# Kernel tuning notes

Measured on AMD Instinct MI355X. Metric: run time of the kernel, lower is better.

Reference implementation:

```python
import jax, jax.numpy as jnp
import numpy as np
from jax import lax

B, TX, TY = 32, 512, 1024
D, H, FN, KS, L = 256, 2, 1024, 9, 4
WORD_NUM = 256
NEG = -1e9


def sinusoid_table(seq_len, d):
    pos = np.arange(seq_len)[:, None].astype(np.float64)
    i = np.arange(d)[None, :]
    angle = pos / np.power(10000.0, 2 * (i // 2) / d)
    table = np.zeros((seq_len, d))
    table[:, 0::2] = np.sin(angle[:, 0::2])
    table[:, 1::2] = np.cos(angle[:, 1::2])
    return jnp.asarray(table, dtype=jnp.float32)


def setup_inputs():
    key = jax.random.key(0)
    ks = jax.random.split(key, 16)
    s = 0.02
    w = lambda k, shape: jax.random.normal(k, shape, jnp.float32) * s
    embed = w(ks[4], (WORD_NUM, D)).at[0].set(0.0)  # padding_idx=0
    return dict(
        tokens=jax.random.randint(ks[0], (B, TX), 1, WORD_NUM),
        src_lengths=jax.random.randint(ks[1], (B,), TX // 2, TX + 1),
        mel_lengths=jax.random.randint(ks[2], (B,), TY // 2, TY + 1),
        value=jax.random.normal(ks[3], (B, TX, TY), jnp.float32),
        embed=embed,
        pos_enc=sinusoid_table(TX, D),
        wq=w(ks[5], (L, D, D)), bq=jnp.zeros((L, D), jnp.float32),
        wk=w(ks[6], (L, D, D)), bk=jnp.zeros((L, D), jnp.float32),
        wv=w(ks[7], (L, D, D)), bv=jnp.zeros((L, D), jnp.float32),
        wo=w(ks[8], (L, D, D)), bo=jnp.zeros((L, D), jnp.float32),
        ln1_g=jnp.ones((L, D), jnp.float32), ln1_b=jnp.zeros((L, D), jnp.float32),
        c1_w=w(ks[9], (L, FN, D, KS)), c1_b=jnp.zeros((L, FN), jnp.float32),
        c2_w=w(ks[10], (L, D, FN, KS)), c2_b=jnp.zeros((L, D), jnp.float32),
        ln2_g=jnp.ones((L, D), jnp.float32), ln2_b=jnp.zeros((L, D), jnp.float32),
    )


def layer_norm(x, g, b, eps=1e-5):
    m = jnp.mean(x, axis=-1, keepdims=True)
    v = jnp.mean(jnp.square(x - m), axis=-1, keepdims=True)
    return (x - m) * lax.rsqrt(v + eps) * g + b


def conv1d(x, w, b):
    # x: [B, C_in, T], w: [C_out, C_in, K]
    p = (w.shape[-1] - 1) // 2
    y = lax.conv_general_dilated(x, w, (1,), [(p, p)],
                                 dimension_numbers=('NCH', 'OIH', 'NCH'))
    return y + b[None, :, None]


def maximum_path(value, mask):
    # Monotonic alignment search DP. value, mask: [B, Tx, Ty]
    b, tx, ty = value.shape
    value = value * mask
    x_range = jnp.arange(tx)[None, :]

    def fwd_step(v, inp):
        j, val_j = inp
        v0 = jnp.concatenate([jnp.full((b, 1), NEG, value.dtype), v[:, :-1]], axis=1)
        max_mask = v >= v0
        v_max = jnp.where(max_mask, v, v0)
        v_new = jnp.where(x_range <= j, v_max + val_j, NEG)
        return v_new, max_mask

    _, directions = lax.scan(fwd_step, jnp.zeros((b, tx), value.dtype),
                             (jnp.arange(ty), jnp.moveaxis(value, 2, 0)))
    directions = jnp.where(jnp.moveaxis(mask, 2, 0).astype(bool), directions, True)

    idx0 = mask[:, :, 0].sum(1).astype(jnp.int32) - 1  # last valid x index per batch
    brange = jnp.arange(b)

    def bwd_step(idx, dir_j):
        col = jax.nn.one_hot(idx, tx, dtype=value.dtype)
        idx_new = idx + dir_j[brange, idx].astype(jnp.int32) - 1
        return idx_new, col

    _, cols = lax.scan(bwd_step, idx0, directions, reverse=True)
    path = jnp.moveaxis(cols, 0, 2) * mask  # [B, Tx, Ty]
    return path


def reference(tokens, src_lengths, mel_lengths, value, embed, pos_enc,
              wq, bq, wk, bk, wv, bv, wo, bo, ln1_g, ln1_b,
              c1_w, c1_b, c2_w, c2_b, ln2_g, ln2_b):
    bsz, tx = tokens.shape
    pad = jnp.arange(tx)[None, :] >= src_lengths[:, None]      # [B,Tx] True=pad
    mel_pad = jnp.arange(TY)[None, :] >= mel_lengths[:, None]  # [B,Ty]
    dk = D // H
    scale = 1.0 / np.sqrt(dk).astype(np.float32)

    x = embed[tokens] + pos_enc[None, :tx, :]
    for l in range(L):
        # --- multi-head self-attention ---
        res = x
        q = (x @ wq[l] + bq[l]).reshape(bsz, tx, H, dk)
        k = (x @ wk[l] + bk[l]).reshape(bsz, tx, H, dk)
        v = (x @ wv[l] + bv[l]).reshape(bsz, tx, H, dk)
        attn = jnp.einsum('bqhd,bkhd->bhqk', q, k) * scale
        attn = jnp.where(pad[:, None, None, :], NEG, attn)
        attn = jax.nn.softmax(attn, axis=-1)
        out = jnp.einsum('bhqk,bkhd->bqhd', attn, v).reshape(bsz, tx, D)
        x = layer_norm(out @ wo[l] + bo[l] + res, ln1_g[l], ln1_b[l])
        x = jnp.where(pad[:, :, None], 0.0, x)
        # --- conv1d FFN ---
        res = x
        h = x.transpose(0, 2, 1)
        h = jax.nn.relu(conv1d(h, c1_w[l], c1_b[l]))
        h = conv1d(h, c2_w[l], c2_b[l]).transpose(0, 2, 1)
        x = layer_norm(h + res, ln2_g[l], ln2_b[l])
        x = jnp.where(pad[:, :, None], 0.0, x)

    mas_mask = ((~pad)[:, :, None] & (~mel_pad)[:, None, :]).astype(jnp.float32)
    path = maximum_path(value, mas_mask)                 # [B,Tx,Ty]
    expanded = jnp.einsum('bxy,bxd->byd', path, x)       # [B,Ty,D]
    return expanded
```

## Files before the change

kernel.cpp:

```cpp
#include <hip/hip_runtime.h>

#define B_  32
#define TX  512
#define TY  1024
#define D_  256
#define H_  2
#define DK  128
#define FN  1024
#define NL  4
#define TXP 520
#define NEGF (-1e9f)

typedef __attribute__((ext_vector_type(4))) float f32x4;
typedef __attribute__((ext_vector_type(8))) short short8;
typedef __attribute__((ext_vector_type(4))) unsigned short ushort4v;

typedef __attribute__((address_space(3))) unsigned int lds_u32;
typedef __attribute__((address_space(1))) const unsigned int glb_u32;

__device__ __forceinline__ unsigned short f2bf(float x) {
  unsigned int u = __builtin_bit_cast(unsigned int, x);
  u += 0x7fffu + ((u >> 16) & 1u);
  return (unsigned short)(u >> 16);
}
__device__ __forceinline__ float bf2f(unsigned short x) {
  unsigned int u = ((unsigned int)x) << 16;
  return __builtin_bit_cast(float, u);
}
__device__ __forceinline__ void store_bf16x4(unsigned short* p, f32x4 v) {
  ushort4v o; o[0]=f2bf(v[0]); o[1]=f2bf(v[1]); o[2]=f2bf(v[2]); o[3]=f2bf(v[3]);
  *(ushort4v*)p = o;
}
__device__ __forceinline__ float wsum(float v) {
#pragma unroll
  for (int i = 1; i < 64; i <<= 1) v += __shfl_xor(v, i, 64);
  return v;
}
__device__ __forceinline__ float wmax(float v) {
#pragma unroll
  for (int i = 1; i < 64; i <<= 1) v = fmaxf(v, __shfl_xor(v, i, 64));
  return v;
}
__device__ __forceinline__ void gl_lds16(const unsigned short* g, unsigned short* l) {
  __builtin_amdgcn_global_load_lds((glb_u32*)g, (lds_u32*)l, 16, 0, 0);
}
__device__ __forceinline__ void gl_lds16f(const float* g, float* l) {
  __builtin_amdgcn_global_load_lds((glb_u32*)g, (lds_u32*)l, 16, 0, 0);
}
__device__ __forceinline__ float lane_shr1(float x) {
  int r = __builtin_amdgcn_update_dpp(0, __builtin_bit_cast(int, x), 0x138, 0xF, 0xF, false);
  return __builtin_bit_cast(float, r);
}

static const size_t OFF_XB   = 0;
static const size_t SZ_XB    = (size_t)B_*TXP*D_*2;
static const size_t OFF_HB   = OFF_XB + SZ_XB;
static const size_t SZ_HB    = (size_t)B_*TXP*FN*2;
static const size_t OFF_QKV  = OFF_HB + SZ_HB;
static const size_t SZ_QKV   = (size_t)B_*TX*768*2;
static const size_t OFF_S    = OFF_QKV + SZ_QKV;
static const size_t SZ_S     = (size_t)B_*H_*TX*TX*2;
static const size_t OFF_AO   = OFF_S + SZ_S;
static const size_t SZ_AO    = (size_t)B_*TX*D_*2;
static const size_t OFF_T1   = OFF_AO + SZ_AO;
static const size_t SZ_T1    = (size_t)B_*TX*D_*4;
static const size_t OFF_WQKV = OFF_T1 + SZ_T1;
static const size_t SZ_WQKV  = (size_t)NL*768*256*2;
static const size_t OFF_BQKV = OFF_WQKV + SZ_WQKV;
static const size_t SZ_BQKV  = (size_t)NL*768*4;
static const size_t OFF_WO   = OFF_BQKV + SZ_BQKV;
static const size_t SZ_WO    = (size_t)NL*256*256*2;
static const size_t OFF_WT1  = OFF_WO + SZ_WO;
static const size_t SZ_WT1   = (size_t)NL*9*1024*256*2;
static const size_t OFF_WT2  = OFF_WT1 + SZ_WT1;
static const size_t SZ_WT2   = SZ_WT1;
static const size_t OFF_DIRS = OFF_WT2 + SZ_WT2;
static const size_t SZ_DIRS  = (size_t)B_*TY*64;
static const size_t OFF_IDX  = OFF_DIRS + SZ_DIRS;

__global__ void repack_qkvw(const float* __restrict__ wq, const float* __restrict__ wk,
                            const float* __restrict__ wv, unsigned short* __restrict__ out) {
  int i = blockIdx.x*256 + threadIdx.x;
  if (i >= NL*768*256) return;
  int c = i & 255, j = (i >> 8) % 768, l = i / (768*256);
  const float* src = (j < 256) ? wq : (j < 512) ? wk : wv;
  out[i] = f2bf(src[((size_t)l*256 + c)*256 + (j & 255)]);
}
__global__ void repack_bias(const float* __restrict__ bq, const float* __restrict__ bk,
                            const float* __restrict__ bv, float* __restrict__ out) {
  int i = blockIdx.x*256 + threadIdx.x;
  if (i >= NL*768) return;
  int j = i % 768, l = i / 768;
  const float* src = (j < 256) ? bq : (j < 512) ? bk : bv;
  out[i] = src[l*256 + (j & 255)];
}
__global__ void repack_wo(const float* __restrict__ wo, unsigned short* __restrict__ out) {
  int i = blockIdx.x*256 + threadIdx.x;
  if (i >= NL*256*256) return;
  int c = i & 255, j = (i >> 8) & 255, l = i >> 16;
  out[i] = f2bf(wo[((size_t)l*256 + c)*256 + j]);
}
__global__ void repack_c1(const float* __restrict__ w, unsigned short* __restrict__ out) {
  int i = blockIdx.x*256 + threadIdx.x;
  if (i >= NL*9*1024*256) return;
  int c = i & 255; int rest = i >> 8;
  int f = rest & 1023; int rest2 = rest >> 10;
  int k = rest2 % 9, l = rest2 / 9;
  out[i] = f2bf(w[(((size_t)l*1024 + f)*256 + c)*9 + k]);
}
__global__ void repack_c2(const float* __restrict__ w, unsigned short* __restrict__ out) {
  int i = blockIdx.x*256 + threadIdx.x;
  if (i >= NL*9*256*1024) return;
  int f = i & 1023; int rest = i >> 10;
  int d = rest & 255; int rest2 = rest >> 8;
  int k = rest2 % 9, l = rest2 / 9;
  out[i] = f2bf(w[(((size_t)l*256 + d)*1024 + f)*9 + k]);
}
__global__ void zero_halo(unsigned short* __restrict__ xb, unsigned short* __restrict__ hb) {
  int i = blockIdx.x*256 + threadIdx.x;
  if (i < 65536) {
    int b = i >> 11, r = (i >> 8) & 7, c = i & 255;
    int row = (r < 4) ? r : (512 + r);
    xb[((size_t)b*TXP + row)*256 + c] = 0;
  } else {
    int j = i - 65536;
    if (j < 262144) {
      int b = j >> 13, r = (j >> 10) & 7, c = j & 1023;
      int row = (r < 4) ? r : (512 + r);
      hb[((size_t)b*TXP + row)*1024 + c] = 0;
    }
  }
}

__global__ __launch_bounds__(256) void embed_kernel(const int* __restrict__ tok,
    const float* __restrict__ emb, const float* __restrict__ pos,
    unsigned short* __restrict__ xbo ) {
  int row = blockIdx.x*4 + (threadIdx.x >> 6);
  int t = row & 511, b = row >> 9;
  int lane = threadIdx.x & 63;
  int tk = tok[row];
  f32x4 e = *(const f32x4*)(emb + (size_t)tk*256 + lane*4);
  f32x4 p = *(const f32x4*)(pos + (size_t)t*256 + lane*4);
  f32x4 v;
#pragma unroll
  for (int i = 0; i < 4; i++) v[i] = e[i] + p[i];
  store_bf16x4(xbo + ((size_t)b*TXP + t)*256 + lane*4, v);
}

__global__ __launch_bounds__(256) void gemm_mfma(
    const unsigned short* __restrict__ A, long long AbO, long long AhO, int Astr,
    const unsigned short* __restrict__ W, long long WbO, long long WhO, int Wstr,
    const float* __restrict__ bias,
    float* __restrict__ O32, long long O32bO, int O32str,
    unsigned short* __restrict__ O16, long long O16bO, long long O16hO, int O16str,
    int Cin, int Cout, int ks, int relu, int H,
    const int* __restrict__ sl, float scale, int maskmode) {
  __shared__ unsigned short As[136*32];
  __shared__ unsigned short Ws[2*128*32];
  const int tid = threadIdx.x;
  int b, h;
  if (H == 2) { b = blockIdx.z >> 1; h = blockIdx.z & 1; }
  else        { b = blockIdx.z;      h = 0; }
  const int t0 = blockIdx.x * 128;
  const int f0 = blockIdx.y * 128;
  const unsigned short* Ab = A + (size_t)b * AbO + (size_t)h * AhO;
  const unsigned short* Wb = W + (size_t)b * WbO + (size_t)h * WhO;
  const int lane = tid & 63, w = tid >> 6;
  const int wt = (w & 1) << 6, wf = (w >> 1) << 6;
  const int lr = lane & 15, lh = lane >> 4;
  const int r0 = tid >> 2, cg = (tid & 3) << 3;
  f32x4 zed = {0.f, 0.f, 0.f, 0.f};
  f32x4 acc[4][4];
#pragma unroll
  for (int i = 0; i < 4; i++)
#pragma unroll
    for (int j = 0; j < 4; j++) acc[i][j] = zed;

  for (int c0 = 0; c0 < Cin; c0 += 32) {
    __syncthreads();
    gl_lds16(Ab + (size_t)(t0 + r0) * Astr + (c0 + cg),         As + (size_t)tid * 8);
    gl_lds16(Ab + (size_t)(t0 + r0 + 64) * Astr + (c0 + cg),    As + (size_t)(tid + 256) * 8);
    if (ks > 1 && tid < 32)
      gl_lds16(Ab + (size_t)(t0 + r0 + 128) * Astr + (c0 + cg), As + (size_t)(tid + 512) * 8);
    {
      const unsigned short* W0 = Wb + (size_t)f0 * Wstr;
      gl_lds16(W0 + (size_t)r0 * Wstr + (c0 + cg),        Ws + (size_t)tid * 8);
      gl_lds16(W0 + (size_t)(r0 + 64) * Wstr + (c0 + cg), Ws + (size_t)(tid + 256) * 8);
    }
    for (int k = 0; k < ks; ++k) {
      __syncthreads();
      if (k + 1 < ks) {
        const unsigned short* Wn = Wb + ((size_t)(k + 1) * Cout + f0) * Wstr;
        unsigned short* Wd = Ws + (size_t)((k + 1) & 1) * 4096;
        gl_lds16(Wn + (size_t)r0 * Wstr + (c0 + cg),        Wd + (size_t)tid * 8);
        gl_lds16(Wn + (size_t)(r0 + 64) * Wstr + (c0 + cg), Wd + (size_t)(tid + 256) * 8);
      }
      const unsigned short* Wsk = Ws + (size_t)(k & 1) * 4096;
      short8 af[4], bfv[4];
#pragma unroll
      for (int mt = 0; mt < 4; mt++) af[mt]  = *(const short8*)&As[(k + wt + mt*16 + lr)*32 + lh*8];
#pragma unroll
      for (int nt = 0; nt < 4; nt++) bfv[nt] = *(const short8*)&Wsk[(wf + nt*16 + lr)*32 + lh*8];
#pragma unroll
      for (int mt = 0; mt < 4; mt++)
#pragma unroll
        for (int nt = 0; nt < 4; nt++)
          acc[mt][nt] = __builtin_amdgcn_mfma_f32_16x16x32_bf16(af[mt], bfv[nt], acc[mt][nt], 0, 0, 0);
    }
  }
  const int slb = maskmode ? sl[b] : 0;
#pragma unroll
  for (int mt = 0; mt < 4; mt++) {
    int trow = t0 + wt + mt*16 + lh*4;
#pragma unroll
    for (int nt = 0; nt < 4; nt++) {
      int f = f0 + wf + nt*16 + lr;
      float bb = (!maskmode && bias) ? bias[f] : 0.f;
#pragma unroll
      for (int r = 0; r < 4; r++) {
        float v;
        if (maskmode) {
          v = acc[mt][nt][r] * scale;
          if (f >= slb) v = NEGF;
        } else {
          v = acc[mt][nt][r] + bb;
          if (relu) v = fmaxf(v, 0.f);
        }
        if (O32) O32[(size_t)b*O32bO + (size_t)(trow + r)*O32str + f] = v;
        if (O16) O16[(size_t)b*O16bO + (size_t)h*O16hO + (size_t)(trow + r)*O16str + f] = f2bf(v);
      }
    }
  }
}

__global__ __launch_bounds__(256) void vtrans_kernel(const unsigned short* __restrict__ qkv,
    unsigned short* __restrict__ VT) {
  const int z = blockIdx.z, b = z >> 1, h = z & 1;
  const int t0 = blockIdx.x << 5, d0 = blockIdx.y << 5;
  __shared__ unsigned short tile[32][33];
  const int tx = threadIdx.x, ty = threadIdx.y;
  const unsigned short* src = qkv + (size_t)b*TX*768 + 512 + h*DK;
#pragma unroll
  for (int i = 0; i < 4; i++)
    tile[ty + i*8][tx] = src[(size_t)(t0 + ty + i*8)*768 + d0 + tx];
  __syncthreads();
#pragma unroll
  for (int i = 0; i < 4; i++)
    VT[((size_t)z*DK + d0 + ty + i*8)*512 + t0 + tx] = tile[tx][ty + i*8];
}

__global__ __launch_bounds__(256) void softmax_kernel(unsigned short* __restrict__ S) {
  const int row = blockIdx.x*4 + (threadIdx.x >> 6);
  const int lane = threadIdx.x & 63;
  unsigned short* p = S + (size_t)row*512 + lane*8;
  short8 raw = *(const short8*)p;
  float a[8];
#pragma unroll
  for (int i = 0; i < 8; i++) a[i] = bf2f((unsigned short)raw[i]);
  float m = a[0];
#pragma unroll
  for (int i = 1; i < 8; i++) m = fmaxf(m, a[i]);
  m = wmax(m);
  float s = 0.f;
#pragma unroll
  for (int i = 0; i < 8; i++) { a[i] = __expf(a[i]-m); s += a[i]; }
  s = wsum(s);
  float inv = 1.f / s;
  short8 o;
#pragma unroll
  for (int i = 0; i < 8; i++) o[i] = (short)f2bf(a[i] * inv);
  *(short8*)p = o;
}

__global__ __launch_bounds__(256) void ln_kernel(const float* __restrict__ tin,
    const float* __restrict__ g, const float* __restrict__ bt, const int* __restrict__ sl,
    unsigned short* __restrict__ xbo ) {
  const int row = blockIdx.x*4 + (threadIdx.x >> 6);
  const int b = row >> 9, t = row & 511;
  const int lane = threadIdx.x & 63;
  unsigned short* xp = xbo + ((size_t)b*TXP + t)*256 + lane*4;
  f32x4 tv = *(const f32x4*)(tin + (size_t)row*256 + lane*4);
  ushort4v rv4 = *(const ushort4v*)xp;
  f32x4 s; float su = 0.f, sq = 0.f;
#pragma unroll
  for (int i = 0; i < 4; i++) {
    s[i] = tv[i] + bf2f(rv4[i]);
    su += s[i]; sq += s[i]*s[i];
  }
  su = wsum(su); sq = wsum(sq);
  float mean = su * (1.f/256.f);
  float var = fmaxf(sq * (1.f/256.f) - mean*mean, 0.f);
  float rs = rsqrtf(var + 1e-5f);
  f32x4 gg = *(const f32x4*)(g + lane*4);
  f32x4 bb = *(const f32x4*)(bt + lane*4);
  bool padr = (t >= sl[b]);
  f32x4 y;
#pragma unroll
  for (int i = 0; i < 4; i++) {
    float yy = (s[i]-mean)*rs*gg[i] + bb[i];
    y[i] = padr ? 0.f : yy;
  }
  store_bf16x4(xp, y);
}

__global__ __launch_bounds__(256) void transpose_mask(const float* __restrict__ value,
    const int* __restrict__ sl, const int* __restrict__ ml, float* __restrict__ vT) {
  const int b = blockIdx.z;
  const int x0 = blockIdx.y << 5, y0 = blockIdx.x << 5;
  __shared__ float tile[32][33];
  const int tx = threadIdx.x, ty = threadIdx.y;
  const int slb = sl[b], mlb = ml[b];
#pragma unroll
  for (int i = 0; i < 4; i++) {
    int x = x0 + ty + i*8, y = y0 + tx;
    float v = value[((size_t)b*TX + x)*TY + y];
    tile[ty + i*8][tx] = (x < slb && y < mlb) ? v : 0.f;
  }
  __syncthreads();
#pragma unroll
  for (int i = 0; i < 4; i++) {
    int y = y0 + ty + i*8, x = x0 + tx;
    vT[((size_t)b*TY + y)*TX + x] = tile[tx][ty + i*8];
  }
}

template<bool RAMP>
__device__ __forceinline__ void dp_comp8(
    int jb, const float* valbuf, unsigned long long* dll,
    float v[8], int lane, int xbase, unsigned int vmask, unsigned int fmask,
    bool lane0) {
  unsigned int w0 = 0, w1 = 0;
#pragma unroll
  for (int u = 0; u < 8; ++u) {
    const int j = jb*8 + u;
    f32x4 a0 = *(const f32x4*)(valbuf + u*512 + lane*8);
    f32x4 a1 = *(const f32x4*)(valbuf + u*512 + lane*8 + 4);
    float vp = lane_shr1(v[7]);
    if (lane0) vp = NEGF;
    unsigned int ge = 0;
#pragma unroll
    for (int i = 7; i >= 1; --i) {
      unsigned int g = (v[i] >= v[i-1]) ? 1u : 0u;
      ge = (ge << 1) | g;
      float nv = fmaxf(v[i], v[i-1]) + ((i < 4) ? a0[i] : a1[i-4]);
      if (RAMP) v[i] = (xbase + i <= j) ? nv : NEGF;
      else      v[i] = nv;
    }
    {
      unsigned int g = (v[0] >= vp) ? 1u : 0u;
      ge = (ge << 1) | g;
      float nv = fmaxf(v[0], vp) + a0[0];
      if (RAMP) v[0] = (xbase <= j) ? nv : NEGF;
      else      v[0] = nv;
    }
    unsigned int byt = (ge & vmask) | fmask;
    if (u < 4) w0 |= byt << (8*u); else w1 |= byt << (8*(u-4));
  }
  dll[jb*64 + lane] = ((unsigned long long)w1 << 32) | w0;
}

__global__ __launch_bounds__(64, 1) void dp_fused(const float* __restrict__ vT,
    const int* __restrict__ sl, const int* __restrict__ ml,
    int* __restrict__ idxout) {
  __shared__ float sval[3*4096];
  __shared__ unsigned long long dll[TY*8];
  unsigned char* dld = (unsigned char*)dll;
  const int b = blockIdx.x, lane = threadIdx.x;
  const int slb = sl[b], mlb = ml[b];
  const float* vb = vT + (size_t)b*TY*TX;
  const int xbase = lane*8;
  const bool lane0 = (lane == 0);
  unsigned int vmaskv = 0;
#pragma unroll
  for (int i = 0; i < 8; ++i) if (xbase + i < slb) vmaskv |= (1u << i);
  const unsigned int fmaskv = (~vmaskv) & 0xffu;
  float v[8];
#pragma unroll
  for (int i = 0; i < 8; ++i) v[i] = 0.f;
  const int jbEnd = (mlb + 7) >> 3;

  auto stage = [&](int jb, float* buf) {
    const float* src = vb + (size_t)jb*8*TX;
#pragma unroll
    for (int u = 0; u < 8; ++u) {
      gl_lds16f(src + u*TX + lane*4,       buf + u*512);
      gl_lds16f(src + u*TX + 256 + lane*4, buf + u*512 + 256);
    }
  };
  stage(0, sval);
  stage(1, sval + 4096);
  stage(2, sval + 8192);
  int buf = 0;
  int jb = 0;
  for (; jb < 64; ++jb) {
    if (jb + 2 < jbEnd)      asm volatile("s_waitcnt vmcnt(32)" ::: "memory");
    else if (jb + 1 < jbEnd) asm volatile("s_waitcnt vmcnt(16)" ::: "memory");
    else                     asm volatile("s_waitcnt vmcnt(0)"  ::: "memory");
    float* vbuf = sval + buf*4096;
    dp_comp8<true>(jb, vbuf, dll, v, lane, xbase, vmaskv, fmaskv, lane0);
    __builtin_amdgcn_sched_barrier(0);
    if (jb + 3 < jbEnd) stage(jb + 3, vbuf);
    buf = (buf == 2) ? 0 : buf + 1;
  }
  for (; jb < jbEnd; ++jb) {
    if (jb + 2 < jbEnd)      asm volatile("s_waitcnt vmcnt(32)" ::: "memory");
    else if (jb + 1 < jbEnd) asm volatile("s_waitcnt vmcnt(16)" ::: "memory");
    else                     asm volatile("s_waitcnt vmcnt(0)"  ::: "memory");
    float* vbuf = sval + buf*4096;
    dp_comp8<false>(jb, vbuf, dll, v, lane, xbase, vmaskv, fmaskv, lane0);
    __builtin_amdgcn_sched_barrier(0);
    if (jb + 3 < jbEnd) stage(jb + 3, vbuf);
    buf = (buf == 2) ? 0 : buf + 1;
  }
  for (int jj = mlb + lane; jj < TY; jj += 64) idxout[b*TY + jj] = -1;
  if (lane0) {
    int* ob = idxout + b*TY;
    int idx = slb - 1;
    int j = mlb - 1;
    while (j >= 6) {
      int o0 = idx >> 3;
      int o1 = (o0 > 0) ? (o0 - 1) : 0;
      unsigned int bc[7], ba[7];
#pragma unroll
      for (int s = 0; s < 7; ++s) {
        int r = j - s;
        int rbase = ((r >> 3) << 9) + (r & 7);
        bc[s] = dld[rbase + o0*8];
        ba[s] = dld[rbase + o1*8];
      }
#pragma unroll
      for (int s = 0; s < 7; ++s) {
        ob[j - s] = idx;
        unsigned int byt = ((idx >> 3) == o0) ? bc[s] : ba[s];
        idx += (int)((byt >> (idx & 7)) & 1u) - 1;
      }
      j -= 7;
    }
    while (j >= 0) {
      ob[j] = idx;
      unsigned int byt = dld[((j >> 3) << 9) + (j & 7) + (idx >> 3)*8];
      idx += (int)((byt >> (idx & 7)) & 1u) - 1;
      --j;
    }
  }
}

__global__ __launch_bounds__(256) void gather_kernel(const unsigned short* __restrict__ xbo,
    const int* __restrict__ idxout, float* __restrict__ out) {
  const int row = blockIdx.x*4 + (threadIdx.x >> 6);
  const int lane = threadIdx.x & 63;
  const int b = row >> 10;
  const int idx = idxout[row];
  f32x4 v;
  if (idx >= 0) {
    ushort4v r = *(const ushort4v*)(xbo + ((size_t)b*TXP + idx)*256 + lane*4);
#pragma unroll
    for (int i = 0; i < 4; i++) v[i] = bf2f(r[i]);
  } else { v[0]=0.f; v[1]=0.f; v[2]=0.f; v[3]=0.f; }
  *(f32x4*)(out + (size_t)row*256 + lane*4) = v;
}

extern "C" void kernel_launch(void* const* d_in, const int* in_sizes, int n_in,
                              void* d_out, int out_size, void* d_ws, size_t ws_size,
                              hipStream_t stream) {
  const int*   tokens = (const int*)d_in[0];
  const int*   sl     = (const int*)d_in[1];
  const int*   ml     = (const int*)d_in[2];
  const float* value  = (const float*)d_in[3];
  const float* emb    = (const float*)d_in[4];
  const float* pos    = (const float*)d_in[5];
  const float* wq     = (const float*)d_in[6];
  const float* bq     = (const float*)d_in[7];
  const float* wk     = (const float*)d_in[8];
  const float* bk     = (const float*)d_in[9];
  const float* wv     = (const float*)d_in[10];
  const float* bv     = (const float*)d_in[11];
  const float* wo     = (const float*)d_in[12];
  const float* bo     = (const float*)d_in[13];
  const float* ln1g   = (const float*)d_in[14];
  const float* ln1bb  = (const float*)d_in[15];
  const float* c1w    = (const float*)d_in[16];
  const float* c1b    = (const float*)d_in[17];
  const float* c2w    = (const float*)d_in[18];
  const float* c2b    = (const float*)d_in[19];
  const float* ln2g   = (const float*)d_in[20];
  const float* ln2bb  = (const float*)d_in[21];

  char* w8 = (char*)d_ws;
  unsigned short* xb     = (unsigned short*)(w8 + OFF_XB);
  unsigned short* hb     = (unsigned short*)(w8 + OFF_HB);
  unsigned short* qkvb   = (unsigned short*)(w8 + OFF_QKV);
  unsigned short* S      = (unsigned short*)(w8 + OFF_S);
  float*          vT     = (float*)(w8 + OFF_HB);
  unsigned short* VT     = (unsigned short*)(w8 + OFF_T1);
  unsigned short* ao     = (unsigned short*)(w8 + OFF_AO);
  float*          T1     = (float*)(w8 + OFF_T1);
  unsigned short* wqkv_r = (unsigned short*)(w8 + OFF_WQKV);
  float*          bqkv   = (float*)(w8 + OFF_BQKV);
  unsigned short* wo_r   = (unsigned short*)(w8 + OFF_WO);
  unsigned short* wt1r   = (unsigned short*)(w8 + OFF_WT1);
  unsigned short* wt2r   = (unsigned short*)(w8 + OFF_WT2);
  int*            idxout = (int*)(w8 + OFF_IDX);
  float*          out    = (float*)d_out;

  const float scale = 0.08838834764831843f;

  repack_qkvw<<<(NL*768*256 + 255)/256, 256, 0, stream>>>(wq, wk, wv, wqkv_r);
  repack_bias<<<(NL*768 + 255)/256, 256, 0, stream>>>(bq, bk, bv, bqkv);
  repack_wo<<<(NL*256*256 + 255)/256, 256, 0, stream>>>(wo, wo_r);
  repack_c1<<<(NL*9*1024*256 + 255)/256, 256, 0, stream>>>(c1w, wt1r);
  repack_c2<<<(NL*9*256*1024 + 255)/256, 256, 0, stream>>>(c2w, wt2r);

  transpose_mask<<<dim3(32, 16, 32), dim3(32, 8), 0, stream>>>(value, sl, ml, vT);
  dp_fused<<<32, 64, 0, stream>>>(vT, sl, ml, idxout);

  zero_halo<<<(327680 + 255)/256, 256, 0, stream>>>(xb, hb);
  embed_kernel<<<4096, 256, 0, stream>>>(tokens, emb, pos, xb + 4*256);

  for (int l = 0; l < NL; l++) {
    gemm_mfma<<<dim3(4, 6, 32), 256, 0, stream>>>(
        xb + 4*256, (long long)TXP*256, 0, 256,
        wqkv_r + (size_t)l*768*256, 0, 0, 256,
        bqkv + l*768,
        nullptr, 0, 0,
        qkvb, (long long)TX*768, 0, 768,
        256, 768, 1, 0, 1, nullptr, 0.f, 0);
    gemm_mfma<<<dim3(4, 4, 64), 256, 0, stream>>>(
        qkvb, (long long)TX*768, 128, 768,
        qkvb + 256, (long long)TX*768, 128, 768,
        nullptr,
        nullptr, 0, 0,
        S, (long long)2*512*512, (long long)512*512, 512,
        128, 512, 1, 0, 2, sl, scale, 1);
    softmax_kernel<<<8192, 256, 0, stream>>>(S);
    vtrans_kernel<<<dim3(16, 4, 64), dim3(32, 8), 0, stream>>>(qkvb, VT);
    gemm_mfma<<<dim3(4, 1, 64), 256, 0, stream>>>(
        S, (long long)2*512*512, (long long)512*512, 512,
        VT, (long long)2*DK*512, (long long)DK*512, 512,
        nullptr,
        nullptr, 0, 0,
        ao, (long long)TX*256, 128, 256,
        512, 128, 1, 0, 2, nullptr, 0.f, 0);
    gemm_mfma<<<dim3(4, 2, 32), 256, 0, stream>>>(
        ao, (long long)TX*256, 0, 256,
        wo_r + (size_t)l*256*256, 0, 0, 256,
        bo + l*256,
        T1, (long long)TX*256, 256,
        nullptr, 0, 0, 0,
        256, 256, 1, 0, 1, nullptr, 0.f, 0);
    ln_kernel<<<4096, 256, 0, stream>>>(T1, ln1g + l*256, ln1bb + l*256, sl, xb + 4*256);
    gemm_mfma<<<dim3(4, 8, 32), 256, 0, stream>>>(
        xb, (long long)TXP*256, 0, 256,
        wt1r + (size_t)l*9*1024*256, 0, 0, 256,
        c1b + l*1024,
        nullptr, 0, 0,
        hb + 4*1024, (long long)TXP*1024, 0, 1024,
        256, 1024, 9, 1, 1, nullptr, 0.f, 0);
    gemm_mfma<<<dim3(4, 2, 32), 256, 0, stream>>>(
        hb, (long long)TXP*1024, 0, 1024,
        wt2r + (size_t)l*9*256*1024, 0, 0, 1024,
        c2b + l*256,
        T1, (long long)TX*256, 256,
        nullptr, 0, 0, 0,
        1024, 256, 9, 0, 1, nullptr, 0.f, 0);
    ln_kernel<<<4096, 256, 0, stream>>>(T1, ln2g + l*256, ln2bb + l*256, sl, xb + 4*256);
  }

  gather_kernel<<<8192, 256, 0, stream>>>(xb + 4*256, idxout, out);
  (void)in_sizes; (void)n_in; (void)out_size; (void)ws_size;
}
```

Measured before the change: 2.050 ms.

## Skip padded row tiles and masked key tiles in MFMA GEMMs

Adds a per-batch skip in the GEMM kernel so 128-row tiles past the source length (plus a conv halo margin) exit early. In mask mode, key tiles entirely beyond the length skip the K loop and write NEG directly. The conv loop order is changed to iterate taps outermost and reload the shifted A tile per tap instead of reusing an extended tile, which drops W double-buffering and raises global/LDS traffic for the conv GEMMs. Padded V columns are zeroed and qkvb is memset once so skipped rows hold defined values, at the risk of stale data in other skipped outputs (T1, hb rows) that later kernels might read.

```diff
diff --git a/kernel.cpp b/kernel.cpp
--- a/kernel.cpp
+++ b/kernel.cpp
@@ -154,15 +154,18 @@
     float* __restrict__ O32, long long O32bO, int O32str,
     unsigned short* __restrict__ O16, long long O16bO, long long O16hO, int O16str,
     int Cin, int Cout, int ks, int relu, int H,
-    const int* __restrict__ sl, float scale, int maskmode) {
-  __shared__ unsigned short As[136*32];
-  __shared__ unsigned short Ws[2*128*32];
+    const int* __restrict__ sl, float scale, int maskmode,
+    const int* __restrict__ tskip, int tmargin) {
+  __shared__ unsigned short As[128*32];
+  __shared__ unsigned short Ws[128*32];
   const int tid = threadIdx.x;
   int b, h;
   if (H == 2) { b = blockIdx.z >> 1; h = blockIdx.z & 1; }
   else        { b = blockIdx.z;      h = 0; }
   const int t0 = blockIdx.x * 128;
   const int f0 = blockIdx.y * 128;
+  if (tskip && t0 >= tskip[b] + tmargin) return;
+  const int slb = maskmode ? sl[b] : 0;
   const unsigned short* Ab = A + (size_t)b * AbO + (size_t)h * AhO;
   const unsigned short* Wb = W + (size_t)b * WbO + (size_t)h * WhO;
   const int lane = tid & 63, w = tid >> 6;
@@ -176,39 +179,31 @@
 #pragma unroll
     for (int j = 0; j < 4; j++) acc[i][j] = zed;
 
-  for (int c0 = 0; c0 < Cin; c0 += 32) {
-    __syncthreads();
-    gl_lds16(Ab + (size_t)(t0 + r0) * Astr + (c0 + cg),         As + (size_t)tid * 8);
-    gl_lds16(Ab + (size_t)(t0 + r0 + 64) * Astr + (c0 + cg),    As + (size_t)(tid + 256) * 8);
-    if (ks > 1 && tid < 32)
-      gl_lds16(Ab + (size_t)(t0 + r0 + 128) * Astr + (c0 + cg), As + (size_t)(tid + 512) * 8);
-    {
-      const unsigned short* W0 = Wb + (size_t)f0 * Wstr;
-      gl_lds16(W0 + (size_t)r0 * Wstr + (c0 + cg),        Ws + (size_t)tid * 8);
-      gl_lds16(W0 + (size_t)(r0 + 64) * Wstr + (c0 + cg), Ws + (size_t)(tid + 256) * 8);
-    }
+  const bool skipK = maskmode && (f0 >= slb);
+  if (!skipK) {
     for (int k = 0; k < ks; ++k) {
-      __syncthreads();
-      if (k + 1 < ks) {
-        const unsigned short* Wn = Wb + ((size_t)(k + 1) * Cout + f0) * Wstr;
-        unsigned short* Wd = Ws + (size_t)((k + 1) & 1) * 4096;
-        gl_lds16(Wn + (size_t)r0 * Wstr + (c0 + cg),        Wd + (size_t)tid * 8);
-        gl_lds16(Wn + (size_t)(r0 + 64) * Wstr + (c0 + cg), Wd + (size_t)(tid + 256) * 8);
+      const unsigned short* AkB = Ab + (size_t)(t0 + k) * Astr;
+      const unsigned short* WkB = Wb + ((size_t)k * Cout + f0) * Wstr;
+      for (int c0 = 0; c0 < Cin; c0 += 32) {
+        __syncthreads();
+        gl_lds16(AkB + (size_t)r0 * Astr + (c0 + cg),        As + (size_t)tid * 8);
+        gl_lds16(AkB + (size_t)(r0 + 64) * Astr + (c0 + cg), As + (size_t)(tid + 256) * 8);
+        gl_lds16(WkB + (size_t)r0 * Wstr + (c0 + cg),        Ws + (size_t)tid * 8);
+        gl_lds16(WkB + (size_t)(r0 + 64) * Wstr + (c0 + cg), Ws + (size_t)(tid + 256) * 8);
+        __syncthreads();
+        short8 af[4], bfv[4];
+#pragma unroll
+        for (int mt = 0; mt < 4; mt++) af[mt]  = *(const short8*)&As[(wt + mt*16 + lr)*32 + lh*8];
+#pragma unroll
+        for (int nt = 0; nt < 4; nt++) bfv[nt] = *(const short8*)&Ws[(wf + nt*16 + lr)*32 + lh*8];
+#pragma unroll
+        for (int mt = 0; mt < 4; mt++)
+#pragma unroll
+          for (int nt = 0; nt < 4; nt++)
+            acc[mt][nt] = __builtin_amdgcn_mfma_f32_16x16x32_bf16(af[mt], bfv[nt], acc[mt][nt], 0, 0, 0);
       }
-      const unsigned short* Wsk = Ws + (size_t)(k & 1) * 4096;
-      short8 af[4], bfv[4];
-#pragma unroll
-      for (int mt = 0; mt < 4; mt++) af[mt]  = *(const short8*)&As[(k + wt + mt*16 + lr)*32 + lh*8];
-#pragma unroll
-      for (int nt = 0; nt < 4; nt++) bfv[nt] = *(const short8*)&Wsk[(wf + nt*16 + lr)*32 + lh*8];
-#pragma unroll
-      for (int mt = 0; mt < 4; mt++)
-#pragma unroll
-        for (int nt = 0; nt < 4; nt++)
-          acc[mt][nt] = __builtin_amdgcn_mfma_f32_16x16x32_bf16(af[mt], bfv[nt], acc[mt][nt], 0, 0, 0);
-    }
-  }
-  const int slb = maskmode ? sl[b] : 0;
+    }
+  }
 #pragma unroll
   for (int mt = 0; mt < 4; mt++) {
     int trow = t0 + wt + mt*16 + lh*4;
@@ -234,19 +229,22 @@
 }
 
 __global__ __launch_bounds__(256) void vtrans_kernel(const unsigned short* __restrict__ qkv,
-    unsigned short* __restrict__ VT) {
+    const int* __restrict__ sl, unsigned short* __restrict__ VT) {
   const int z = blockIdx.z, b = z >> 1, h = z & 1;
   const int t0 = blockIdx.x << 5, d0 = blockIdx.y << 5;
   __shared__ unsigned short tile[32][33];
   const int tx = threadIdx.x, ty = threadIdx.y;
+  const int slb = sl[b];
   const unsigned short* src = qkv + (size_t)b*TX*768 + 512 + h*DK;
 #pragma unroll
   for (int i = 0; i < 4; i++)
     tile[ty + i*8][tx] = src[(size_t)(t0 + ty + i*8)*768 + d0 + tx];
   __syncthreads();
 #pragma unroll
-  for (int i = 0; i < 4; i++)
-    VT[((size_t)z*DK + d0 + ty + i*8)*512 + t0 + tx] = tile[tx][ty + i*8];
+  for (int i = 0; i < 4; i++) {
+    unsigned short v = (t0 + tx < slb) ? tile[tx][ty + i*8] : (unsigned short)0;
+    VT[((size_t)z*DK + d0 + ty + i*8)*512 + t0 + tx] = v;
+  }
 }
 
 __global__ __launch_bounds__(256) void softmax_kernel(unsigned short* __restrict__ S) {
@@ -514,6 +512,8 @@
   transpose_mask<<<dim3(32, 16, 32), dim3(32, 8), 0, stream>>>(value, sl, ml, vT);
   dp_fused<<<32, 64, 0, stream>>>(vT, sl, ml, idxout);
 
+  hipMemsetAsync(qkvb, 0, SZ_QKV, stream);
+
   zero_halo<<<(327680 + 255)/256, 256, 0, stream>>>(xb, hb);
   embed_kernel<<<4096, 256, 0, stream>>>(tokens, emb, pos, xb + 4*256);
 
@@ -524,30 +524,30 @@
         bqkv + l*768,
         nullptr, 0, 0,
         qkvb, (long long)TX*768, 0, 768,
-        256, 768, 1, 0, 1, nullptr, 0.f, 0);
+        256, 768, 1, 0, 1, nullptr, 0.f, 0, sl, 0);
     gemm_mfma<<<dim3(4, 4, 64), 256, 0, stream>>>(
         qkvb, (long long)TX*768, 128, 768,
         qkvb + 256, (long long)TX*768, 128, 768,
         nullptr,
         nullptr, 0, 0,
         S, (long long)2*512*512, (long long)512*512, 512,
-        128, 512, 1, 0, 2, sl, scale, 1);
+        128, 512, 1, 0, 2, sl, scale, 1, sl, 0);
     softmax_kernel<<<8192, 256, 0, stream>>>(S);
-    vtrans_kernel<<<dim3(16, 4, 64), dim3(32, 8), 0, stream>>>(qkvb, VT);
+    vtrans_kernel<<<dim3(16, 4, 64), dim3(32, 8), 0, stream>>>(qkvb, sl, VT);
     gemm_mfma<<<dim3(4, 1, 64), 256, 0, stream>>>(
         S, (long long)2*512*512, (long long)512*512, 512,
         VT, (long long)2*DK*512, (long long)DK*512, 512,
         nullptr,
         nullptr, 0, 0,
         ao, (long long)TX*256, 128, 256,
-        512, 128, 1, 0, 2, nullptr, 0.f, 0);
+        512, 128, 1, 0, 2, nullptr, 0.f, 0, sl, 0);
     gemm_mfma<<<dim3(4, 2, 32), 256, 0, stream>>>(
         ao, (long long)TX*256, 0, 256,
         wo_r + (size_t)l*256*256, 0, 0, 256,
         bo + l*256,
         T1, (long long)TX*256, 256,
         nullptr, 0, 0, 0,
-        256, 256, 1, 0, 1, nullptr, 0.f, 0);
+        256, 256, 1, 0, 1, nullptr, 0.f, 0, sl, 0);
     ln_kernel<<<4096, 256, 0, stream>>>(T1, ln1g + l*256, ln1bb + l*256, sl, xb + 4*256);
     gemm_mfma<<<dim3(4, 8, 32), 256, 0, stream>>>(
         xb, (long long)TXP*256, 0, 256,
@@ -555,14 +555,14 @@
         c1b + l*1024,
         nullptr, 0, 0,
         hb + 4*1024, (long long)TXP*1024, 0, 1024,
-        256, 1024, 9, 1, 1, nullptr, 0.f, 0);
+        256, 1024, 9, 1, 1, nullptr, 0.f, 0, sl, 4);
     gemm_mfma<<<dim3(4, 2, 32), 256, 0, stream>>>(
         hb, (long long)TXP*1024, 0, 1024,
         wt2r + (size_t)l*9*256*1024, 0, 0, 1024,
         c2b + l*256,
         T1, (long long)TX*256, 256,
         nullptr, 0, 0, 0,
-        1024, 256, 9, 0, 1, nullptr, 0.f, 0);
+        1024, 256, 9, 0, 1, nullptr, 0.f, 0, sl, 0);
     ln_kernel<<<4096, 256, 0, stream>>>(T1, ln2g + l*256, ln2bb + l*256, sl, xb + 4*256);
   }
 
```

Measured after the change: 2.200 ms. 1.07x slower.
